# Kernel optimization log

Hardware: AMD Instinct MI355X
Metric: run time of the kernel (lower is better)

The kernel has to match this reference:

```python
import jax, jax.numpy as jnp
import numpy as np

N_HEAD = 12
HEAD_DIM = 64
N_EMBD = 768
ATTN_MULT = 0.125
B, T = 2, 2048
NEG_INF = -1e30


def setup_inputs() -> dict:
    key = jax.random.key(0)
    ks = jax.random.split(key, 3)
    x = jax.random.normal(ks[0], (B, T, N_EMBD), dtype=jnp.float32)
    W_attn = jax.random.normal(ks[1], (N_EMBD, 3 * N_HEAD * HEAD_DIM), dtype=jnp.float32) * 0.02
    b_attn = jnp.zeros((3 * N_HEAD * HEAD_DIM,), dtype=jnp.float32)
    W_proj = jax.random.normal(ks[2], (N_HEAD * HEAD_DIM, N_EMBD), dtype=jnp.float32) * 0.02
    b_proj = jnp.zeros((N_EMBD,), dtype=jnp.float32)
    return {"x": x, "W_attn": W_attn, "b_attn": b_attn, "W_proj": W_proj, "b_proj": b_proj}


def reference(x, W_attn, b_attn, W_proj, b_proj):
    Bsz, Tlen, C = x.shape
    H, D = N_HEAD, HEAD_DIM
    qkv = x @ W_attn + b_attn                       # [B,T,3*H*D]
    q, k, v = jnp.split(qkv, 3, axis=-1)
    q = q.reshape(Bsz, Tlen, H, D).transpose(0, 2, 1, 3)   # [B,H,T,D]
    k = k.reshape(Bsz, Tlen, H, D).transpose(0, 2, 1, 3)
    v = v.reshape(Bsz, Tlen, H, D).transpose(0, 2, 1, 3)

    att = jnp.einsum('bhtd,bhsd->bhts', q, k) * ATTN_MULT  # [B,H,T,T]
    causal = jnp.tril(jnp.ones((Tlen, Tlen), dtype=bool))  # [T,T]
    att = jnp.where(causal, att, NEG_INF)

    # selection mask from head 0 (SelectionHeadLinearComboKind.NONE)
    S = jax.nn.relu(att[:, 0:1, :, :])                     # [B,1,T,T]; relu kills -inf
    # protect_bos_token: zero column 0 (key index 0)
    col = jnp.arange(Tlen)
    S = S * (col[None, None, None, :] != 0)
    # prevent_from_masking_myself: zero diagonal
    S = S * (1.0 - jnp.eye(Tlen, dtype=S.dtype))

    # accumulate selection over query (row) axis: ProtectionKind.NONE
    FF = jnp.cumsum(S, axis=-2)                            # [B,1,T,T]
    att = att - FF                                         # broadcast over heads

    p = jax.nn.softmax(att, axis=-1)                       # [B,H,T,T]
    y = jnp.einsum('bhts,bhsd->bhtd', p, v)                # [B,H,T,D]
    y = y.transpose(0, 2, 1, 3).reshape(Bsz, Tlen, H * D)  # [B,T,H*D]
    return y @ W_proj + b_proj
```

## Files before the change

### kernel.cpp

```cpp
#include <hip/hip_runtime.h>
#include <math.h>

#define T 2048
#define NH 12
#define HD 64
#define C3 2304
#define CE 768
#define NB 2

typedef __attribute__((ext_vector_type(8))) short bf16x8;
typedef __attribute__((ext_vector_type(4))) float f32x4;

__device__ inline void bf16split(float a, unsigned short& h, unsigned short& l) {
    unsigned int u = __float_as_uint(a);
    unsigned int r = (u + 0x7FFFu + ((u >> 16) & 1u)) >> 16;
    h = (unsigned short)r;
    float hf = __uint_as_float(r << 16);
    float lo = a - hf;
    unsigned int v = __float_as_uint(lo);
    l = (unsigned short)((v + 0x7FFFu + ((v >> 16) & 1u)) >> 16);
}

__global__ __launch_bounds__(256) void cvt_split_kernel(const float* __restrict__ A,
        unsigned short* __restrict__ H, unsigned short* __restrict__ L) {
    int i = blockIdx.x * 256 + threadIdx.x;
    float4 a0 = *(reinterpret_cast<const float4*>(A) + (size_t)i * 2);
    float4 a1 = *(reinterpret_cast<const float4*>(A) + (size_t)i * 2 + 1);
    float f[8] = {a0.x, a0.y, a0.z, a0.w, a1.x, a1.y, a1.z, a1.w};
    unsigned short h[8], l[8];
    #pragma unroll
    for (int j = 0; j < 8; ++j) bf16split(f[j], h[j], l[j]);
    uint4 hv, lv;
    hv.x = (unsigned)h[0] | ((unsigned)h[1] << 16); hv.y = (unsigned)h[2] | ((unsigned)h[3] << 16);
    hv.z = (unsigned)h[4] | ((unsigned)h[5] << 16); hv.w = (unsigned)h[6] | ((unsigned)h[7] << 16);
    lv.x = (unsigned)l[0] | ((unsigned)l[1] << 16); lv.y = (unsigned)l[2] | ((unsigned)l[3] << 16);
    lv.z = (unsigned)l[4] | ((unsigned)l[5] << 16); lv.w = (unsigned)l[6] | ((unsigned)l[7] << 16);
    reinterpret_cast<uint4*>(H)[i] = hv;
    reinterpret_cast<uint4*>(L)[i] = lv;
}

__global__ __launch_bounds__(256) void cvt_split_T_kernel(const float* __restrict__ W,
        unsigned short* __restrict__ H, unsigned short* __restrict__ L, int K, int N) {
    __shared__ float tile[64][65];
    const int n0 = blockIdx.x * 64, k0 = blockIdx.y * 64;
    const int t = threadIdx.x;
    {
        int r = t >> 2, c4 = (t & 3) * 16;
        #pragma unroll
        for (int u = 0; u < 4; ++u) {
            float4 w = *reinterpret_cast<const float4*>(&W[(size_t)(k0 + r) * N + n0 + c4 + u * 4]);
            tile[r][c4 + u * 4 + 0] = w.x; tile[r][c4 + u * 4 + 1] = w.y;
            tile[r][c4 + u * 4 + 2] = w.z; tile[r][c4 + u * 4 + 3] = w.w;
        }
    }
    __syncthreads();
    {
        int n = t >> 2, kc = (t & 3) * 16;
        unsigned short h[16], l[16];
        #pragma unroll
        for (int j = 0; j < 16; ++j) bf16split(tile[kc + j][n], h[j], l[j]);
        uint4 hv0, hv1, lv0, lv1;
        hv0.x = (unsigned)h[0] | ((unsigned)h[1] << 16);  hv0.y = (unsigned)h[2] | ((unsigned)h[3] << 16);
        hv0.z = (unsigned)h[4] | ((unsigned)h[5] << 16);  hv0.w = (unsigned)h[6] | ((unsigned)h[7] << 16);
        hv1.x = (unsigned)h[8] | ((unsigned)h[9] << 16);  hv1.y = (unsigned)h[10] | ((unsigned)h[11] << 16);
        hv1.z = (unsigned)h[12] | ((unsigned)h[13] << 16); hv1.w = (unsigned)h[14] | ((unsigned)h[15] << 16);
        lv0.x = (unsigned)l[0] | ((unsigned)l[1] << 16);  lv0.y = (unsigned)l[2] | ((unsigned)l[3] << 16);
        lv0.z = (unsigned)l[4] | ((unsigned)l[5] << 16);  lv0.w = (unsigned)l[6] | ((unsigned)l[7] << 16);
        lv1.x = (unsigned)l[8] | ((unsigned)l[9] << 16);  lv1.y = (unsigned)l[10] | ((unsigned)l[11] << 16);
        lv1.z = (unsigned)l[12] | ((unsigned)l[13] << 16); lv1.w = (unsigned)l[14] | ((unsigned)l[15] << 16);
        size_t o = (size_t)(n0 + n) * K + k0 + kc;
        reinterpret_cast<uint4*>(&H[o])[0] = hv0; reinterpret_cast<uint4*>(&H[o])[1] = hv1;
        reinterpret_cast<uint4*>(&L[o])[0] = lv0; reinterpret_cast<uint4*>(&L[o])[1] = lv1;
    }
}

__global__ __launch_bounds__(256) void cvt_kv_k_kernel(const float* __restrict__ qkv,
        unsigned short* __restrict__ Kh, unsigned short* __restrict__ Kl) {
    int t = blockIdx.x * 256 + threadIdx.x;
    int dg = t & 7;
    int s = (t >> 3) & (T - 1);
    int bh = t >> 14;
    int b = bh / NH, h = bh % NH;
    const float* src = qkv + (size_t)(b * T + s) * C3 + 768 + h * 64 + dg * 8;
    float4 a0 = *reinterpret_cast<const float4*>(src);
    float4 a1 = *reinterpret_cast<const float4*>(src + 4);
    float f[8] = {a0.x, a0.y, a0.z, a0.w, a1.x, a1.y, a1.z, a1.w};
    unsigned short hh[8], ll[8];
    #pragma unroll
    for (int j = 0; j < 8; ++j) bf16split(f[j], hh[j], ll[j]);
    uint4 hv, lv;
    hv.x = (unsigned)hh[0] | ((unsigned)hh[1] << 16); hv.y = (unsigned)hh[2] | ((unsigned)hh[3] << 16);
    hv.z = (unsigned)hh[4] | ((unsigned)hh[5] << 16); hv.w = (unsigned)hh[6] | ((unsigned)hh[7] << 16);
    lv.x = (unsigned)ll[0] | ((unsigned)ll[1] << 16); lv.y = (unsigned)ll[2] | ((unsigned)ll[3] << 16);
    lv.z = (unsigned)ll[4] | ((unsigned)ll[5] << 16); lv.w = (unsigned)ll[6] | ((unsigned)ll[7] << 16);
    size_t o = ((size_t)bh * T + s) * 64 + dg * 8;
    *reinterpret_cast<uint4*>(&Kh[o]) = hv;
    *reinterpret_cast<uint4*>(&Kl[o]) = lv;
}

__global__ __launch_bounds__(256) void cvt_kv_vt_kernel(const float* __restrict__ qkv,
        unsigned short* __restrict__ Vh, unsigned short* __restrict__ Vl) {
    __shared__ float tile[64][65];
    const int s0 = blockIdx.x * 64;
    const int bh = blockIdx.y;
    const int b = bh / NH, h = bh % NH;
    const int tid = threadIdx.x;
    {
        int r = tid >> 2, c0 = (tid & 3) * 16;
        const float* src = qkv + (size_t)(b * T + s0 + r) * C3 + 1536 + h * 64 + c0;
        #pragma unroll
        for (int u = 0; u < 4; ++u) {
            float4 w = *reinterpret_cast<const float4*>(src + u * 4);
            tile[r][c0 + u * 4 + 0] = w.x; tile[r][c0 + u * 4 + 1] = w.y;
            tile[r][c0 + u * 4 + 2] = w.z; tile[r][c0 + u * 4 + 3] = w.w;
        }
    }
    __syncthreads();
    {
        int d = tid >> 2, cs = (tid & 3) * 16;
        unsigned short hh[16], ll[16];
        #pragma unroll
        for (int j = 0; j < 16; ++j) bf16split(tile[cs + j][d], hh[j], ll[j]);
        uint4 hv0, hv1, lv0, lv1;
        hv0.x = (unsigned)hh[0] | ((unsigned)hh[1] << 16);  hv0.y = (unsigned)hh[2] | ((unsigned)hh[3] << 16);
        hv0.z = (unsigned)hh[4] | ((unsigned)hh[5] << 16);  hv0.w = (unsigned)hh[6] | ((unsigned)hh[7] << 16);
        hv1.x = (unsigned)hh[8] | ((unsigned)hh[9] << 16);  hv1.y = (unsigned)hh[10] | ((unsigned)hh[11] << 16);
        hv1.z = (unsigned)hh[12] | ((unsigned)hh[13] << 16); hv1.w = (unsigned)hh[14] | ((unsigned)hh[15] << 16);
        lv0.x = (unsigned)ll[0] | ((unsigned)ll[1] << 16);  lv0.y = (unsigned)ll[2] | ((unsigned)ll[3] << 16);
        lv0.z = (unsigned)ll[4] | ((unsigned)ll[5] << 16);  lv0.w = (unsigned)ll[6] | ((unsigned)ll[7] << 16);
        lv1.x = (unsigned)ll[8] | ((unsigned)ll[9] << 16);  lv1.y = (unsigned)ll[10] | ((unsigned)ll[11] << 16);
        lv1.z = (unsigned)ll[12] | ((unsigned)ll[13] << 16); lv1.w = (unsigned)ll[14] | ((unsigned)ll[15] << 16);
        size_t o = ((size_t)bh * 64 + d) * T + s0 + cs;
        reinterpret_cast<uint4*>(&Vh[o])[0] = hv0; reinterpret_cast<uint4*>(&Vh[o])[1] = hv1;
        reinterpret_cast<uint4*>(&Vl[o])[0] = lv0; reinterpret_cast<uint4*>(&Vl[o])[1] = lv1;
    }
}

#define LDST 40
__global__ __launch_bounds__(256) void gemm_mfma_kernel(
        const unsigned short* __restrict__ Ah, const unsigned short* __restrict__ Al,
        const unsigned short* __restrict__ Bh, const unsigned short* __restrict__ Bl,
        const float* __restrict__ bias, float* __restrict__ Cm,
        int M, int N, int K) {
    __shared__ unsigned short lA[2][128 * LDST];
    __shared__ unsigned short lB[2][128 * LDST];
    const int tid = threadIdx.x;
    const int bm = blockIdx.y * 128, bn = blockIdx.x * 128;
    const int lane = tid & 63, wid = tid >> 6;
    const int wr = wid >> 1, wc = wid & 1;
    f32x4 acc[4][4];
    #pragma unroll
    for (int i = 0; i < 4; ++i)
        #pragma unroll
        for (int j = 0; j < 4; ++j) acc[i][j] = (f32x4){0.f, 0.f, 0.f, 0.f};
    const int srow = tid >> 2, sk8 = (tid & 3) * 8;
    const int arb = wr * 64 + (lane & 15);
    const int brb = wc * 64 + (lane & 15);
    const int koff = (lane >> 4) * 8;
    for (int k0 = 0; k0 < K; k0 += 32) {
        __syncthreads();
        #pragma unroll
        for (int c = 0; c < 2; ++c) {
            int row = srow + 64 * c;
            uint4 va = *reinterpret_cast<const uint4*>(&Ah[(size_t)(bm + row) * K + k0 + sk8]);
            uint4 vb = *reinterpret_cast<const uint4*>(&Al[(size_t)(bm + row) * K + k0 + sk8]);
            uint4 vc = *reinterpret_cast<const uint4*>(&Bh[(size_t)(bn + row) * K + k0 + sk8]);
            uint4 vd = *reinterpret_cast<const uint4*>(&Bl[(size_t)(bn + row) * K + k0 + sk8]);
            *reinterpret_cast<uint4*>(&lA[0][row * LDST + sk8]) = va;
            *reinterpret_cast<uint4*>(&lA[1][row * LDST + sk8]) = vb;
            *reinterpret_cast<uint4*>(&lB[0][row * LDST + sk8]) = vc;
            *reinterpret_cast<uint4*>(&lB[1][row * LDST + sk8]) = vd;
        }
        __syncthreads();
        bf16x8 fa[2][4], fb[2][4];
        #pragma unroll
        for (int fi = 0; fi < 4; ++fi) {
            fa[0][fi] = *reinterpret_cast<const bf16x8*>(&lA[0][(arb + fi * 16) * LDST + koff]);
            fa[1][fi] = *reinterpret_cast<const bf16x8*>(&lA[1][(arb + fi * 16) * LDST + koff]);
            fb[0][fi] = *reinterpret_cast<const bf16x8*>(&lB[0][(brb + fi * 16) * LDST + koff]);
            fb[1][fi] = *reinterpret_cast<const bf16x8*>(&lB[1][(brb + fi * 16) * LDST + koff]);
        }
        #pragma unroll
        for (int fi = 0; fi < 4; ++fi)
            #pragma unroll
            for (int fj = 0; fj < 4; ++fj) {
                acc[fi][fj] = __builtin_amdgcn_mfma_f32_16x16x32_bf16(fa[0][fi], fb[0][fj], acc[fi][fj], 0, 0, 0);
                acc[fi][fj] = __builtin_amdgcn_mfma_f32_16x16x32_bf16(fa[0][fi], fb[1][fj], acc[fi][fj], 0, 0, 0);
                acc[fi][fj] = __builtin_amdgcn_mfma_f32_16x16x32_bf16(fa[1][fi], fb[0][fj], acc[fi][fj], 0, 0, 0);
            }
    }
    #pragma unroll
    for (int fj = 0; fj < 4; ++fj) {
        int col = bn + wc * 64 + fj * 16 + (lane & 15);
        float bv = bias[col];
        #pragma unroll
        for (int fi = 0; fi < 4; ++fi) {
            int row0 = bm + wr * 64 + fi * 16 + (lane >> 4) * 4;
            #pragma unroll
            for (int p = 0; p < 4; ++p)
                Cm[(size_t)(row0 + p) * N + col] = acc[fi][fj][p] + bv;
        }
    }
}

__global__ __launch_bounds__(256) void gemm_bias_kernel(
        const float* __restrict__ A, const float* __restrict__ B,
        const float* __restrict__ bias, float* __restrict__ Cm,
        int M, int N, int K) {
    __shared__ float As[16][64];
    __shared__ float Bs[16][68];
    const int tid = threadIdx.x;
    const int ty = tid >> 4, tx = tid & 15;
    const int bm = blockIdx.y * 64, bn = blockIdx.x * 64;
    float acc[4][4] = {};
    for (int k0 = 0; k0 < K; k0 += 16) {
        {
            int r = tid >> 2;
            int kk = (tid & 3) * 4;
            float4 a = *reinterpret_cast<const float4*>(&A[(size_t)(bm + r) * K + k0 + kk]);
            As[kk + 0][r] = a.x; As[kk + 1][r] = a.y; As[kk + 2][r] = a.z; As[kk + 3][r] = a.w;
        }
        {
            int kk = tid >> 4;
            int c = (tid & 15) * 4;
            *reinterpret_cast<float4*>(&Bs[kk][c]) =
                *reinterpret_cast<const float4*>(&B[(size_t)(k0 + kk) * N + bn + c]);
        }
        __syncthreads();
        #pragma unroll
        for (int kk = 0; kk < 16; ++kk) {
            float4 a4 = *reinterpret_cast<const float4*>(&As[kk][ty * 4]);
            float4 b4 = *reinterpret_cast<const float4*>(&Bs[kk][tx * 4]);
            float av[4] = {a4.x, a4.y, a4.z, a4.w};
            float bv[4] = {b4.x, b4.y, b4.z, b4.w};
            #pragma unroll
            for (int i = 0; i < 4; ++i)
                #pragma unroll
                for (int j = 0; j < 4; ++j)
                    acc[i][j] = fmaf(av[i], bv[j], acc[i][j]);
        }
        __syncthreads();
    }
    #pragma unroll
    for (int i = 0; i < 4; ++i) {
        int row = bm + ty * 4 + i;
        #pragma unroll
        for (int j = 0; j < 4; ++j) {
            int col = bn + tx * 4 + j;
            Cm[(size_t)row * N + col] = acc[i][j] + bias[col];
        }
    }
}

__global__ __launch_bounds__(256) void s0_kernel(const float* __restrict__ qkv,
                                                 float* __restrict__ S) {
    const int kb = blockIdx.x * 64, qb = blockIdx.y * 64, b = blockIdx.z;
    const int tid = threadIdx.x, ty = tid >> 4, tx = tid & 15;
    float* Sb = S + (size_t)b * T * T;
    if (kb > qb) {
        #pragma unroll
        for (int i = 0; i < 4; ++i) {
            int row = qb + ty * 4 + i;
            float4 z = {0.f, 0.f, 0.f, 0.f};
            *reinterpret_cast<float4*>(&Sb[(size_t)row * T + kb + tx * 4]) = z;
        }
        return;
    }
    __shared__ float Qt[64][68];
    __shared__ float Kt[64][68];
    {
        int r = tid >> 2;
        int c0 = (tid & 3) * 16;
        const float* qrow = qkv + (size_t)(b * T + qb + r) * C3 + 0;
        const float* krow = qkv + (size_t)(b * T + kb + r) * C3 + 768;
        #pragma unroll
        for (int u = 0; u < 4; ++u) {
            float4 q4 = *reinterpret_cast<const float4*>(&qrow[c0 + u * 4]);
            float4 k4 = *reinterpret_cast<const float4*>(&krow[c0 + u * 4]);
            int d = c0 + u * 4;
            Qt[d + 0][r] = q4.x; Qt[d + 1][r] = q4.y; Qt[d + 2][r] = q4.z; Qt[d + 3][r] = q4.w;
            Kt[d + 0][r] = k4.x; Kt[d + 1][r] = k4.y; Kt[d + 2][r] = k4.z; Kt[d + 3][r] = k4.w;
        }
    }
    __syncthreads();
    float acc[4][4] = {};
    #pragma unroll
    for (int d = 0; d < 64; ++d) {
        float4 qv = *reinterpret_cast<const float4*>(&Qt[d][ty * 4]);
        float4 kv = *reinterpret_cast<const float4*>(&Kt[d][tx * 4]);
        float qa[4] = {qv.x, qv.y, qv.z, qv.w};
        float ka[4] = {kv.x, kv.y, kv.z, kv.w};
        #pragma unroll
        for (int i = 0; i < 4; ++i)
            #pragma unroll
            for (int j = 0; j < 4; ++j)
                acc[i][j] = fmaf(qa[i], ka[j], acc[i][j]);
    }
    #pragma unroll
    for (int i = 0; i < 4; ++i) {
        int t = qb + ty * 4 + i;
        float o[4];
        #pragma unroll
        for (int j = 0; j < 4; ++j) {
            int s = kb + tx * 4 + j;
            float v = acc[i][j] * 0.125f;
            o[j] = (s >= 1 && s < t) ? fmaxf(v, 0.0f) : 0.0f;
        }
        float4 o4 = {o[0], o[1], o[2], o[3]};
        *reinterpret_cast<float4*>(&Sb[(size_t)t * T + kb + tx * 4]) = o4;
    }
}

__global__ __launch_bounds__(256) void colsum_kernel(const float* __restrict__ S,
                                                     float* __restrict__ Psum) {
    int s = blockIdx.x * 256 + threadIdx.x;
    int j = blockIdx.y, b = blockIdx.z;
    const float* Sb = S + (size_t)b * T * T;
    float sum = 0.f;
    for (int r = 0; r < 64; ++r) sum += Sb[(size_t)(j * 64 + r) * T + s];
    Psum[((size_t)b * 32 + j) * T + s] = sum;
}

__global__ __launch_bounds__(256) void scanseg_kernel(float* __restrict__ Psum) {
    int s = blockIdx.x * 256 + threadIdx.x;
    int b = blockIdx.y;
    float run = 0.f;
    for (int j = 0; j < 32; ++j) {
        size_t idx = ((size_t)b * 32 + j) * T + s;
        float v = Psum[idx];
        Psum[idx] = run;
        run += v;
    }
}

__global__ __launch_bounds__(256) void ffscan_kernel(float* __restrict__ S,
                                                     const float* __restrict__ Psum) {
    int s = blockIdx.x * 256 + threadIdx.x;
    int j = blockIdx.y, b = blockIdx.z;
    float run = Psum[((size_t)b * 32 + j) * T + s];
    float* Sb = S + (size_t)b * T * T;
    for (int r = 0; r < 64; ++r) {
        size_t idx = (size_t)(j * 64 + r) * T + s;
        run += Sb[idx];
        Sb[idx] = run;
    }
}

#define FST 72
__global__ __launch_bounds__(256) void flash_mfma_kernel(
        const float* __restrict__ qkv,
        const unsigned short* __restrict__ Kh, const unsigned short* __restrict__ Kl,
        const unsigned short* __restrict__ Vth, const unsigned short* __restrict__ Vtl,
        const float* __restrict__ FF, float* __restrict__ Y,
        float* __restrict__ PO, float* __restrict__ PML, int split) {
    const int hb = blockIdx.x;
    const int h = hb % NH, b = hb / NH;
    int qt, kt0, kt1, mode;
    if (split) {
        const int u = blockIdx.y;
        if (u < 16)      { qt = 16 + u; kt0 = 0;  kt1 = 16;     mode = 1; }
        else if (u < 32) { qt = 31 - u; kt0 = 0;  kt1 = qt + 1; mode = 0; }
        else             { qt = 63 - u; kt0 = 16; kt1 = qt + 1; mode = 2; }
    } else {
        qt = 31 - blockIdx.y; kt0 = 0; kt1 = qt + 1; mode = 0;
    }
    const int qb = qt * 64;
    const int tid = threadIdx.x;
    const int lane = tid & 63, w = tid >> 6;
    const int fr = lane & 15, fg = lane >> 4;
    __shared__ unsigned short KP[2][64 * FST];
    __shared__ unsigned short Vt[2][64 * FST];

    bf16x8 qh[2], ql[2];
    #pragma unroll
    for (int ks = 0; ks < 2; ++ks) {
        const float* qp = qkv + (size_t)(b * T + qb + w * 16 + fr) * C3 + h * 64 + ks * 32 + fg * 8;
        float4 q0 = *reinterpret_cast<const float4*>(qp);
        float4 q1 = *reinterpret_cast<const float4*>(qp + 4);
        float qf[8] = {q0.x, q0.y, q0.z, q0.w, q1.x, q1.y, q1.z, q1.w};
        #pragma unroll
        for (int e = 0; e < 8; ++e) {
            unsigned short hh, ll;
            bf16split(qf[e], hh, ll);
            qh[ks][e] = (short)hh; ql[ks][e] = (short)ll;
        }
    }

    float m[4], l[4];
    f32x4 Oacc[4];
    #pragma unroll
    for (int p = 0; p < 4; ++p) { m[p] = -1e30f; l[p] = 0.f; }
    #pragma unroll
    for (int fd = 0; fd < 4; ++fd) Oacc[fd] = (f32x4){0.f, 0.f, 0.f, 0.f};

    const float* FFb = FF + (size_t)b * T * T;
    const int sr = tid >> 2, sc0 = (tid & 3) * 16;

    for (int kt = kt0; kt < kt1; ++kt) {
        const int kb = kt * 64;
        __syncthreads();
        {
            const unsigned short* ksrc = Kh + ((size_t)hb * T + kb + sr) * 64 + sc0;
            const unsigned short* ksrl = Kl + ((size_t)hb * T + kb + sr) * 64 + sc0;
            const unsigned short* vsrc = Vth + ((size_t)hb * 64 + sr) * T + kb + sc0;
            const unsigned short* vsrl = Vtl + ((size_t)hb * 64 + sr) * T + kb + sc0;
            uint4 k0v = reinterpret_cast<const uint4*>(ksrc)[0];
            uint4 k1v = reinterpret_cast<const uint4*>(ksrc)[1];
            uint4 k2v = reinterpret_cast<const uint4*>(ksrl)[0];
            uint4 k3v = reinterpret_cast<const uint4*>(ksrl)[1];
            uint4 v0v = reinterpret_cast<const uint4*>(vsrc)[0];
            uint4 v1v = reinterpret_cast<const uint4*>(vsrc)[1];
            uint4 v2v = reinterpret_cast<const uint4*>(vsrl)[0];
            uint4 v3v = reinterpret_cast<const uint4*>(vsrl)[1];
            *reinterpret_cast<uint4*>(&KP[0][sr * FST + sc0 + 0]) = k0v;
            *reinterpret_cast<uint4*>(&KP[0][sr * FST + sc0 + 8]) = k1v;
            *reinterpret_cast<uint4*>(&KP[1][sr * FST + sc0 + 0]) = k2v;
            *reinterpret_cast<uint4*>(&KP[1][sr * FST + sc0 + 8]) = k3v;
            *reinterpret_cast<uint4*>(&Vt[0][sr * FST + sc0 + 0]) = v0v;
            *reinterpret_cast<uint4*>(&Vt[0][sr * FST + sc0 + 8]) = v1v;
            *reinterpret_cast<uint4*>(&Vt[1][sr * FST + sc0 + 0]) = v2v;
            *reinterpret_cast<uint4*>(&Vt[1][sr * FST + sc0 + 8]) = v3v;
        }
        __syncthreads();
        f32x4 qk[4];
        #pragma unroll
        for (int fj = 0; fj < 4; ++fj) qk[fj] = (f32x4){0.f, 0.f, 0.f, 0.f};
        #pragma unroll
        for (int ks = 0; ks < 2; ++ks) {
            bf16x8 kbh[4], kbl[4];
            #pragma unroll
            for (int fj = 0; fj < 4; ++fj) {
                kbh[fj] = *reinterpret_cast<const bf16x8*>(&KP[0][(fj * 16 + fr) * FST + ks * 32 + fg * 8]);
                kbl[fj] = *reinterpret_cast<const bf16x8*>(&KP[1][(fj * 16 + fr) * FST + ks * 32 + fg * 8]);
            }
            #pragma unroll
            for (int fj = 0; fj < 4; ++fj) {
                qk[fj] = __builtin_amdgcn_mfma_f32_16x16x32_bf16(qh[ks], kbh[fj], qk[fj], 0, 0, 0);
                qk[fj] = __builtin_amdgcn_mfma_f32_16x16x32_bf16(qh[ks], kbl[fj], qk[fj], 0, 0, 0);
                qk[fj] = __builtin_amdgcn_mfma_f32_16x16x32_bf16(ql[ks], kbh[fj], qk[fj], 0, 0, 0);
            }
        }
        float sc[4][4];
        #pragma unroll
        for (int p = 0; p < 4; ++p) {
            int t = qb + w * 16 + fg * 4 + p;
            #pragma unroll
            for (int fj = 0; fj < 4; ++fj) {
                int s = kb + fj * 16 + fr;
                float v = qk[fj][p] * 0.125f - FFb[(size_t)t * T + s];
                sc[fj][p] = (s <= t) ? v : -1e30f;
            }
        }
        #pragma unroll
        for (int p = 0; p < 4; ++p) {
            float tm = fmaxf(fmaxf(sc[0][p], sc[1][p]), fmaxf(sc[2][p], sc[3][p]));
            tm = fmaxf(tm, __shfl_xor(tm, 1));
            tm = fmaxf(tm, __shfl_xor(tm, 2));
            tm = fmaxf(tm, __shfl_xor(tm, 4));
            tm = fmaxf(tm, __shfl_xor(tm, 8));
            float mn = fmaxf(m[p], tm);
            float scale = __expf(m[p] - mn);
            float rs = 0.f;
            #pragma unroll
            for (int fj = 0; fj < 4; ++fj) {
                float pe = __expf(sc[fj][p] - mn);
                sc[fj][p] = pe; rs += pe;
            }
            rs += __shfl_xor(rs, 1); rs += __shfl_xor(rs, 2);
            rs += __shfl_xor(rs, 4); rs += __shfl_xor(rs, 8);
            l[p] = l[p] * scale + rs;
            m[p] = mn;
            #pragma unroll
            for (int fd = 0; fd < 4; ++fd) Oacc[fd][p] *= scale;
        }
        __syncthreads();
        #pragma unroll
        for (int p = 0; p < 4; ++p) {
            int qrow = w * 16 + fg * 4 + p;
            #pragma unroll
            for (int fj = 0; fj < 4; ++fj) {
                unsigned short hh, ll;
                bf16split(sc[fj][p], hh, ll);
                KP[0][qrow * FST + fj * 16 + fr] = hh;
                KP[1][qrow * FST + fj * 16 + fr] = ll;
            }
        }
        __syncthreads();
        #pragma unroll
        for (int ks = 0; ks < 2; ++ks) {
            bf16x8 pah = *reinterpret_cast<const bf16x8*>(&KP[0][(w * 16 + fr) * FST + ks * 32 + fg * 8]);
            bf16x8 pal = *reinterpret_cast<const bf16x8*>(&KP[1][(w * 16 + fr) * FST + ks * 32 + fg * 8]);
            bf16x8 vbh[4], vbl[4];
            #pragma unroll
            for (int fd = 0; fd < 4; ++fd) {
                vbh[fd] = *reinterpret_cast<const bf16x8*>(&Vt[0][(fd * 16 + fr) * FST + ks * 32 + fg * 8]);
                vbl[fd] = *reinterpret_cast<const bf16x8*>(&Vt[1][(fd * 16 + fr) * FST + ks * 32 + fg * 8]);
            }
            #pragma unroll
            for (int fd = 0; fd < 4; ++fd) {
                Oacc[fd] = __builtin_amdgcn_mfma_f32_16x16x32_bf16(pah, vbh[fd], Oacc[fd], 0, 0, 0);
                Oacc[fd] = __builtin_amdgcn_mfma_f32_16x16x32_bf16(pah, vbl[fd], Oacc[fd], 0, 0, 0);
                Oacc[fd] = __builtin_amdgcn_mfma_f32_16x16x32_bf16(pal, vbh[fd], Oacc[fd], 0, 0, 0);
            }
        }
    }
    if (mode == 0) {
        #pragma unroll
        for (int p = 0; p < 4; ++p) {
            int t = qb + w * 16 + fg * 4 + p;
            float inv = 1.f / l[p];
            float* Yrow = Y + (size_t)(b * T + t) * CE + h * 64;
            #pragma unroll
            for (int fd = 0; fd < 4; ++fd)
                Yrow[fd * 16 + fr] = Oacc[fd][p] * inv;
        }
    } else {
        const int pidx = (b * NH + h) * 16 + (qt - 16);
        float* Ob  = PO  + (size_t)(mode - 1) * (NB * NH * 16 * 4096) + (size_t)pidx * 4096;
        float* mlb = PML + (size_t)(mode - 1) * (NB * NH * 16 * 128)  + (size_t)pidx * 128;
        #pragma unroll
        for (int p = 0; p < 4; ++p) {
            int rr = w * 16 + fg * 4 + p;
            #pragma unroll
            for (int fd = 0; fd < 4; ++fd)
                Ob[rr * 64 + fd * 16 + fr] = Oacc[fd][p];
            if (fr == 0) { mlb[rr] = m[p]; mlb[64 + rr] = l[p]; }
        }
    }
}

__global__ __launch_bounds__(256) void flash_kernel(const float* __restrict__ qkv,
                                                    const float* __restrict__ FF,
                                                    float* __restrict__ Y,
                                                    float* __restrict__ PO,
                                                    float* __restrict__ PML,
                                                    int split) {
    const int hb = blockIdx.x;
    const int h = hb % NH, b = hb / NH;
    int qt, kt0, kt1, mode;
    if (split) {
        const int u = blockIdx.y;
        if (u < 16)      { qt = 16 + u; kt0 = 0;  kt1 = 16;     mode = 1; }
        else if (u < 32) { qt = 31 - u; kt0 = 0;  kt1 = qt + 1; mode = 0; }
        else             { qt = 63 - u; kt0 = 16; kt1 = qt + 1; mode = 2; }
    } else {
        qt = 31 - blockIdx.y; kt0 = 0; kt1 = qt + 1; mode = 0;
    }
    const int qb = qt * 64;
    const int tid = threadIdx.x, ty = tid >> 4, tx = tid & 15;
    __shared__ float Qt[64][68];
    __shared__ float KtPs[64][68];
    __shared__ float Vs[64][68];
    const int r = tid >> 2, c0 = (tid & 3) * 16;
    {
        const float* qrow = qkv + (size_t)(b * T + qb + r) * C3 + h * 64;
        #pragma unroll
        for (int u = 0; u < 4; ++u) {
            float4 q4 = *reinterpret_cast<const float4*>(&qrow[c0 + u * 4]);
            int d = c0 + u * 4;
            Qt[d + 0][r] = q4.x; Qt[d + 1][r] = q4.y; Qt[d + 2][r] = q4.z; Qt[d + 3][r] = q4.w;
        }
    }
    float m[4], l[4], O[4][4];
    #pragma unroll
    for (int i = 0; i < 4; ++i) {
        m[i] = -1e30f; l[i] = 0.f;
        #pragma unroll
        for (int j = 0; j < 4; ++j) O[i][j] = 0.f;
    }
    const float* FFb = FF + (size_t)b * T * T;
    for (int kt = kt0; kt < kt1; ++kt) {
        const int kb = kt * 64;
        __syncthreads();
        {
            const float* krow = qkv + (size_t)(b * T + kb + r) * C3 + 768 + h * 64;
            const float* vrow = qkv + (size_t)(b * T + kb + r) * C3 + 1536 + h * 64;
            #pragma unroll
            for (int u = 0; u < 4; ++u) {
                float4 k4 = *reinterpret_cast<const float4*>(&krow[c0 + u * 4]);
                int d = c0 + u * 4;
                KtPs[d + 0][r] = k4.x; KtPs[d + 1][r] = k4.y;
                KtPs[d + 2][r] = k4.z; KtPs[d + 3][r] = k4.w;
                *reinterpret_cast<float4*>(&Vs[r][c0 + u * 4]) =
                    *reinterpret_cast<const float4*>(&vrow[c0 + u * 4]);
            }
        }
        __syncthreads();
        float sc[4][4] = {};
        #pragma unroll
        for (int d = 0; d < 64; ++d) {
            float4 qv = *reinterpret_cast<const float4*>(&Qt[d][ty * 4]);
            float4 kv = *reinterpret_cast<const float4*>(&KtPs[d][tx * 4]);
            float qa[4] = {qv.x, qv.y, qv.z, qv.w};
            float ka[4] = {kv.x, kv.y, kv.z, kv.w};
            #pragma unroll
            for (int i = 0; i < 4; ++i)
                #pragma unroll
                for (int j = 0; j < 4; ++j)
                    sc[i][j] = fmaf(qa[i], ka[j], sc[i][j]);
        }
        #pragma unroll
        for (int i = 0; i < 4; ++i) {
            int t = qb + ty * 4 + i;
            float4 f4 = *reinterpret_cast<const float4*>(&FFb[(size_t)t * T + kb + tx * 4]);
            float fv[4] = {f4.x, f4.y, f4.z, f4.w};
            #pragma unroll
            for (int j = 0; j < 4; ++j) {
                int s = kb + tx * 4 + j;
                float v = sc[i][j] * 0.125f - fv[j];
                sc[i][j] = (s <= t) ? v : -1e30f;
            }
        }
        #pragma unroll
        for (int i = 0; i < 4; ++i) {
            float tm = fmaxf(fmaxf(sc[i][0], sc[i][1]), fmaxf(sc[i][2], sc[i][3]));
            tm = fmaxf(tm, __shfl_xor(tm, 1));
            tm = fmaxf(tm, __shfl_xor(tm, 2));
            tm = fmaxf(tm, __shfl_xor(tm, 4));
            tm = fmaxf(tm, __shfl_xor(tm, 8));
            float mn = fmaxf(m[i], tm);
            float scale = __expf(m[i] - mn);
            float rs = 0.f;
            #pragma unroll
            for (int j = 0; j < 4; ++j) {
                float p = __expf(sc[i][j] - mn);
                sc[i][j] = p; rs += p;
            }
            rs += __shfl_xor(rs, 1); rs += __shfl_xor(rs, 2);
            rs += __shfl_xor(rs, 4); rs += __shfl_xor(rs, 8);
            l[i] = l[i] * scale + rs;
            m[i] = mn;
            #pragma unroll
            for (int j = 0; j < 4; ++j) O[i][j] *= scale;
        }
        __syncthreads();
        #pragma unroll
        for (int i = 0; i < 4; ++i) {
            float4 p4 = {sc[i][0], sc[i][1], sc[i][2], sc[i][3]};
            *reinterpret_cast<float4*>(&KtPs[ty * 4 + i][tx * 4]) = p4;
        }
        __syncthreads();
        #pragma unroll
        for (int j4 = 0; j4 < 16; ++j4) {
            float pv[4][4];
            #pragma unroll
            for (int i = 0; i < 4; ++i) {
                float4 t4 = *reinterpret_cast<const float4*>(&KtPs[ty * 4 + i][j4 * 4]);
                pv[i][0] = t4.x; pv[i][1] = t4.y; pv[i][2] = t4.z; pv[i][3] = t4.w;
            }
            #pragma unroll
            for (int jj = 0; jj < 4; ++jj) {
                float4 v4 = *reinterpret_cast<const float4*>(&Vs[j4 * 4 + jj][tx * 4]);
                float vv[4] = {v4.x, v4.y, v4.z, v4.w};
                #pragma unroll
                for (int i = 0; i < 4; ++i)
                    #pragma unroll
                    for (int dd = 0; dd < 4; ++dd)
                        O[i][dd] = fmaf(pv[i][jj], vv[dd], O[i][dd]);
            }
        }
    }
    if (mode == 0) {
        #pragma unroll
        for (int i = 0; i < 4; ++i) {
            int t = qb + ty * 4 + i;
            float inv = 1.f / l[i];
            float4 o4 = {O[i][0] * inv, O[i][1] * inv, O[i][2] * inv, O[i][3] * inv};
            *reinterpret_cast<float4*>(&Y[(size_t)(b * T + t) * CE + h * 64 + tx * 4]) = o4;
        }
    } else {
        const int pidx = (b * NH + h) * 16 + (qt - 16);
        float* Ob  = PO  + (size_t)(mode - 1) * (NB * NH * 16 * 4096) + (size_t)pidx * 4096;
        float* mlb = PML + (size_t)(mode - 1) * (NB * NH * 16 * 128)  + (size_t)pidx * 128;
        #pragma unroll
        for (int i = 0; i < 4; ++i) {
            int rr = ty * 4 + i;
            float4 o4 = {O[i][0], O[i][1], O[i][2], O[i][3]};
            *reinterpret_cast<float4*>(&Ob[rr * 64 + tx * 4]) = o4;
            if (tx == 0) { mlb[rr] = m[i]; mlb[64 + rr] = l[i]; }
        }
    }
}

__global__ __launch_bounds__(256) void merge_kernel(const float* __restrict__ PO,
                                                    const float* __restrict__ PML,
                                                    float* __restrict__ Y) {
    const int p = blockIdx.x;
    const int q16 = p & 15;
    const int hb = p >> 4;
    const int h = hb % NH, b = hb / NH;
    const int qt = 16 + q16;
    const float* O0  = PO  + (size_t)p * 4096;
    const float* O1  = PO  + (size_t)(NB * NH * 16) * 4096 + (size_t)p * 4096;
    const float* ml0 = PML + (size_t)p * 128;
    const float* ml1 = PML + (size_t)(NB * NH * 16) * 128  + (size_t)p * 128;
    const int tid = threadIdx.x;
    const int r = tid >> 2, c0 = (tid & 3) * 16;
    float m0 = ml0[r], l0 = ml0[64 + r];
    float m1 = ml1[r], l1 = ml1[64 + r];
    float M  = fmaxf(m0, m1);
    float a0 = __expf(m0 - M), a1 = __expf(m1 - M);
    float inv = 1.f / (a0 * l0 + a1 * l1);
    const int t = qt * 64 + r;
    float* Yrow = Y + (size_t)(b * T + t) * CE + h * 64;
    #pragma unroll
    for (int u = 0; u < 4; ++u) {
        float4 x0 = *reinterpret_cast<const float4*>(&O0[r * 64 + c0 + u * 4]);
        float4 x1 = *reinterpret_cast<const float4*>(&O1[r * 64 + c0 + u * 4]);
        float4 y;
        y.x = (a0 * x0.x + a1 * x1.x) * inv;
        y.y = (a0 * x0.y + a1 * x1.y) * inv;
        y.z = (a0 * x0.z + a1 * x1.z) * inv;
        y.w = (a0 * x0.w + a1 * x1.w) * inv;
        *reinterpret_cast<float4*>(&Yrow[c0 + u * 4]) = y;
    }
}

extern "C" void kernel_launch(void* const* d_in, const int* in_sizes, int n_in,
                              void* d_out, int out_size, void* d_ws, size_t ws_size,
                              hipStream_t stream) {
    const float* x      = (const float*)d_in[0];
    const float* W_attn = (const float*)d_in[1];
    const float* b_attn = (const float*)d_in[2];
    const float* W_proj = (const float*)d_in[3];
    const float* b_proj = (const float*)d_in[4];
    float* out = (float*)d_out;

    char* ws = (char*)d_ws;
    const size_t QKV_BYTES = (size_t)NB * T * C3 * 4;
    const size_t S_BYTES   = (size_t)NB * T * T * 4;
    const size_t P_BYTES   = (size_t)NB * 32 * T * 4;
    const size_t Y_BYTES   = (size_t)NB * T * CE * 4;
    const size_t PO_BYTES  = (size_t)2 * NB * NH * 16 * 4096 * 4;
    const size_t PML_BYTES = (size_t)2 * NB * NH * 16 * 128 * 4;
    const size_t PLANE_X   = (size_t)NB * T * CE * 2;
    const size_t PLANE_WA  = (size_t)C3 * CE * 2;
    const size_t PLANE_WP  = (size_t)CE * CE * 2;
    const size_t PLANE_KV  = (size_t)NB * NH * T * 64 * 2;

    const size_t U_OFF  = QKV_BYTES + S_BYTES + P_BYTES + Y_BYTES;
    const size_t U_SIZE = PO_BYTES + PML_BYTES;
    const size_t W_OFF  = U_OFF + U_SIZE;
    const size_t KV_OFF = W_OFF + 2 * PLANE_WA + 2 * PLANE_WP;

    float* qkv  = (float*)ws;
    float* S    = (float*)(ws + QKV_BYTES);
    float* Psum = (float*)(ws + QKV_BYTES + S_BYTES);
    float* Yb   = (float*)(ws + QKV_BYTES + S_BYTES + P_BYTES);
    float* PO   = (float*)(ws + U_OFF);
    float* PML  = (float*)(ws + U_OFF + PO_BYTES);
    unsigned short* Xh  = (unsigned short*)(ws + U_OFF);
    unsigned short* Xl  = (unsigned short*)(ws + U_OFF + PLANE_X);
    unsigned short* Yh  = Xh;
    unsigned short* Yl  = Xl;
    unsigned short* WAh = (unsigned short*)(ws + W_OFF);
    unsigned short* WAl = (unsigned short*)(ws + W_OFF + PLANE_WA);
    unsigned short* WPh = (unsigned short*)(ws + W_OFF + 2 * PLANE_WA);
    unsigned short* WPl = (unsigned short*)(ws + W_OFF + 2 * PLANE_WA + PLANE_WP);
    unsigned short* Khp = (unsigned short*)(ws + KV_OFF);
    unsigned short* Klp = (unsigned short*)(ws + KV_OFF + PLANE_KV);
    unsigned short* VTh = (unsigned short*)(ws + KV_OFF + 2 * PLANE_KV);
    unsigned short* VTl = (unsigned short*)(ws + KV_OFF + 3 * PLANE_KV);

    const size_t NEED_SPLIT = U_OFF + U_SIZE;
    const size_t NEED_MFMA  = KV_OFF;
    const size_t NEED_KV    = KV_OFF + 4 * PLANE_KV;
    const int split = (ws_size >= NEED_SPLIT) ? 1 : 0;
    const int mfma  = (ws_size >= NEED_MFMA) ? 1 : 0;
    const int kv    = (ws_size >= NEED_KV) ? 1 : 0;

    const int M = NB * T;

    if (mfma) {
        cvt_split_T_kernel<<<dim3(C3 / 64, CE / 64), 256, 0, stream>>>(W_attn, WAh, WAl, CE, C3);
        cvt_split_T_kernel<<<dim3(CE / 64, CE / 64), 256, 0, stream>>>(W_proj, WPh, WPl, CE, CE);
        cvt_split_kernel<<<dim3((M * CE / 8) / 256), 256, 0, stream>>>(x, Xh, Xl);
        gemm_mfma_kernel<<<dim3(C3 / 128, M / 128), 256, 0, stream>>>(Xh, Xl, WAh, WAl, b_attn, qkv, M, C3, CE);
    } else {
        gemm_bias_kernel<<<dim3(C3 / 64, M / 64), 256, 0, stream>>>(x, W_attn, b_attn, qkv, M, C3, CE);
    }
    s0_kernel<<<dim3(T / 64, T / 64, NB), 256, 0, stream>>>(qkv, S);
    colsum_kernel<<<dim3(T / 256, 32, NB), 256, 0, stream>>>(S, Psum);
    scanseg_kernel<<<dim3(T / 256, NB), 256, 0, stream>>>(Psum);
    ffscan_kernel<<<dim3(T / 256, 32, NB), 256, 0, stream>>>(S, Psum);
    if (kv) {
        cvt_kv_k_kernel<<<dim3((NB * NH * T * 8) / 256), 256, 0, stream>>>(qkv, Khp, Klp);
        cvt_kv_vt_kernel<<<dim3(T / 64, NB * NH), 256, 0, stream>>>(qkv, VTh, VTl);
        if (split) {
            flash_mfma_kernel<<<dim3(NB * NH, 48), 256, 0, stream>>>(qkv, Khp, Klp, VTh, VTl, S, Yb, PO, PML, 1);
            merge_kernel<<<dim3(NB * NH * 16), 256, 0, stream>>>(PO, PML, Yb);
        } else {
            flash_mfma_kernel<<<dim3(NB * NH, 32), 256, 0, stream>>>(qkv, Khp, Klp, VTh, VTl, S, Yb, PO, PML, 0);
        }
    } else if (split) {
        flash_kernel<<<dim3(NB * NH, 48), 256, 0, stream>>>(qkv, S, Yb, PO, PML, 1);
        merge_kernel<<<dim3(NB * NH * 16), 256, 0, stream>>>(PO, PML, Yb);
    } else {
        flash_kernel<<<dim3(NB * NH, 32), 256, 0, stream>>>(qkv, S, Yb, PO, PML, 0);
    }
    if (mfma) {
        cvt_split_kernel<<<dim3((M * CE / 8) / 256), 256, 0, stream>>>(Yb, Yh, Yl);
        gemm_mfma_kernel<<<dim3(CE / 128, M / 128), 256, 0, stream>>>(Yh, Yl, WPh, WPl, b_proj, out, M, CE, CE);
    } else {
        gemm_bias_kernel<<<dim3(CE / 64, M / 64), 256, 0, stream>>>(Yb, W_proj, b_proj, out, M, CE, CE);
    }
}
```

Baseline: 293.2 us.

## Precompute Q bf16 split, use MFMA for head-0 scores, finer flash KV chunking

```diff
diff --git a/kernel.cpp b/kernel.cpp
--- a/kernel.cpp
+++ b/kernel.cpp
@@ -74,28 +74,39 @@
     }
 }
 
-__global__ __launch_bounds__(256) void cvt_kv_k_kernel(const float* __restrict__ qkv,
+__global__ __launch_bounds__(256) void cvt_qk_kernel(const float* __restrict__ qkv,
+        unsigned short* __restrict__ Qh, unsigned short* __restrict__ Ql,
         unsigned short* __restrict__ Kh, unsigned short* __restrict__ Kl) {
     int t = blockIdx.x * 256 + threadIdx.x;
     int dg = t & 7;
     int s = (t >> 3) & (T - 1);
     int bh = t >> 14;
     int b = bh / NH, h = bh % NH;
-    const float* src = qkv + (size_t)(b * T + s) * C3 + 768 + h * 64 + dg * 8;
-    float4 a0 = *reinterpret_cast<const float4*>(src);
-    float4 a1 = *reinterpret_cast<const float4*>(src + 4);
-    float f[8] = {a0.x, a0.y, a0.z, a0.w, a1.x, a1.y, a1.z, a1.w};
-    unsigned short hh[8], ll[8];
-    #pragma unroll
-    for (int j = 0; j < 8; ++j) bf16split(f[j], hh[j], ll[j]);
-    uint4 hv, lv;
-    hv.x = (unsigned)hh[0] | ((unsigned)hh[1] << 16); hv.y = (unsigned)hh[2] | ((unsigned)hh[3] << 16);
-    hv.z = (unsigned)hh[4] | ((unsigned)hh[5] << 16); hv.w = (unsigned)hh[6] | ((unsigned)hh[7] << 16);
-    lv.x = (unsigned)ll[0] | ((unsigned)ll[1] << 16); lv.y = (unsigned)ll[2] | ((unsigned)ll[3] << 16);
-    lv.z = (unsigned)ll[4] | ((unsigned)ll[5] << 16); lv.w = (unsigned)ll[6] | ((unsigned)ll[7] << 16);
+    const float* qs = qkv + (size_t)(b * T + s) * C3 + h * 64 + dg * 8;
+    const float* ks = qs + 768;
     size_t o = ((size_t)bh * T + s) * 64 + dg * 8;
-    *reinterpret_cast<uint4*>(&Kh[o]) = hv;
-    *reinterpret_cast<uint4*>(&Kl[o]) = lv;
+    #pragma unroll
+    for (int which = 0; which < 2; ++which) {
+        const float* src = (which == 0) ? qs : ks;
+        float4 a0 = *reinterpret_cast<const float4*>(src);
+        float4 a1 = *reinterpret_cast<const float4*>(src + 4);
+        float f[8] = {a0.x, a0.y, a0.z, a0.w, a1.x, a1.y, a1.z, a1.w};
+        unsigned short hh[8], ll[8];
+        #pragma unroll
+        for (int j = 0; j < 8; ++j) bf16split(f[j], hh[j], ll[j]);
+        uint4 hv, lv;
+        hv.x = (unsigned)hh[0] | ((unsigned)hh[1] << 16); hv.y = (unsigned)hh[2] | ((unsigned)hh[3] << 16);
+        hv.z = (unsigned)hh[4] | ((unsigned)hh[5] << 16); hv.w = (unsigned)hh[6] | ((unsigned)hh[7] << 16);
+        lv.x = (unsigned)ll[0] | ((unsigned)ll[1] << 16); lv.y = (unsigned)ll[2] | ((unsigned)ll[3] << 16);
+        lv.z = (unsigned)ll[4] | ((unsigned)ll[5] << 16); lv.w = (unsigned)ll[6] | ((unsigned)ll[7] << 16);
+        if (which == 0) {
+            *reinterpret_cast<uint4*>(&Qh[o]) = hv;
+            *reinterpret_cast<uint4*>(&Ql[o]) = lv;
+        } else {
+            *reinterpret_cast<uint4*>(&Kh[o]) = hv;
+            *reinterpret_cast<uint4*>(&Kl[o]) = lv;
+        }
+    }
 }
 
 __global__ __launch_bounds__(256) void cvt_kv_vt_kernel(const float* __restrict__ qkv,
@@ -252,6 +263,79 @@
     }
 }
 
+#define FST 72
+
+__global__ __launch_bounds__(256) void s0_mfma_kernel(
+        const unsigned short* __restrict__ Qh, const unsigned short* __restrict__ Ql,
+        const unsigned short* __restrict__ Kh, const unsigned short* __restrict__ Kl,
+        float* __restrict__ S) {
+    const int kb = blockIdx.x * 64, qb = blockIdx.y * 64, b = blockIdx.z;
+    const int tid = threadIdx.x;
+    float* Sb = S + (size_t)b * T * T;
+    if (kb > qb) {
+        const int ty = tid >> 4, tx = tid & 15;
+        #pragma unroll
+        for (int i = 0; i < 4; ++i) {
+            float4 z = {0.f, 0.f, 0.f, 0.f};
+            *reinterpret_cast<float4*>(&Sb[(size_t)(qb + ty * 4 + i) * T + kb + tx * 4]) = z;
+        }
+        return;
+    }
+    const int lane = tid & 63, w = tid >> 6;
+    const int fr = lane & 15, fg = lane >> 4;
+    __shared__ unsigned short Ks[2][64 * FST];
+    const int hb0 = b * NH;
+    {
+        const int sr = tid >> 2, sc0 = (tid & 3) * 16;
+        const unsigned short* kh = Kh + ((size_t)hb0 * T + kb + sr) * 64 + sc0;
+        const unsigned short* kl = Kl + ((size_t)hb0 * T + kb + sr) * 64 + sc0;
+        uint4 a0 = reinterpret_cast<const uint4*>(kh)[0];
+        uint4 a1 = reinterpret_cast<const uint4*>(kh)[1];
+        uint4 b0 = reinterpret_cast<const uint4*>(kl)[0];
+        uint4 b1 = reinterpret_cast<const uint4*>(kl)[1];
+        *reinterpret_cast<uint4*>(&Ks[0][sr * FST + sc0 + 0]) = a0;
+        *reinterpret_cast<uint4*>(&Ks[0][sr * FST + sc0 + 8]) = a1;
+        *reinterpret_cast<uint4*>(&Ks[1][sr * FST + sc0 + 0]) = b0;
+        *reinterpret_cast<uint4*>(&Ks[1][sr * FST + sc0 + 8]) = b1;
+    }
+    bf16x8 qh[2], ql[2];
+    #pragma unroll
+    for (int ks = 0; ks < 2; ++ks) {
+        size_t qo = ((size_t)hb0 * T + qb + w * 16 + fr) * 64 + ks * 32 + fg * 8;
+        qh[ks] = *reinterpret_cast<const bf16x8*>(&Qh[qo]);
+        ql[ks] = *reinterpret_cast<const bf16x8*>(&Ql[qo]);
+    }
+    __syncthreads();
+    f32x4 qk[4];
+    #pragma unroll
+    for (int fj = 0; fj < 4; ++fj) qk[fj] = (f32x4){0.f, 0.f, 0.f, 0.f};
+    #pragma unroll
+    for (int ks = 0; ks < 2; ++ks) {
+        bf16x8 kbh[4], kbl[4];
+        #pragma unroll
+        for (int fj = 0; fj < 4; ++fj) {
+            kbh[fj] = *reinterpret_cast<const bf16x8*>(&Ks[0][(fj * 16 + fr) * FST + ks * 32 + fg * 8]);
+            kbl[fj] = *reinterpret_cast<const bf16x8*>(&Ks[1][(fj * 16 + fr) * FST + ks * 32 + fg * 8]);
+        }
+        #pragma unroll
+        for (int fj = 0; fj < 4; ++fj) {
+            qk[fj] = __builtin_amdgcn_mfma_f32_16x16x32_bf16(qh[ks], kbh[fj], qk[fj], 0, 0, 0);
+            qk[fj] = __builtin_amdgcn_mfma_f32_16x16x32_bf16(qh[ks], kbl[fj], qk[fj], 0, 0, 0);
+            qk[fj] = __builtin_amdgcn_mfma_f32_16x16x32_bf16(ql[ks], kbh[fj], qk[fj], 0, 0, 0);
+        }
+    }
+    #pragma unroll
+    for (int p = 0; p < 4; ++p) {
+        int t = qb + w * 16 + fg * 4 + p;
+        #pragma unroll
+        for (int fj = 0; fj < 4; ++fj) {
+            int s = kb + fj * 16 + fr;
+            float v = qk[fj][p] * 0.125f;
+            Sb[(size_t)t * T + s] = (s >= 1 && s < t) ? fmaxf(v, 0.0f) : 0.0f;
+        }
+    }
+}
+
 __global__ __launch_bounds__(256) void s0_kernel(const float* __restrict__ qkv,
                                                  float* __restrict__ S) {
     const int kb = blockIdx.x * 64, qb = blockIdx.y * 64, b = blockIdx.z;
@@ -346,23 +430,42 @@
     }
 }
 
-#define FST 72
+__device__ inline int chunk_base_fn(int qt) {
+    int base = 0;
+    for (int q = 8; q < qt; ++q) base += (q + 8) >> 3;
+    return base;
+}
+
 __global__ __launch_bounds__(256) void flash_mfma_kernel(
-        const float* __restrict__ qkv,
+        const unsigned short* __restrict__ Qh, const unsigned short* __restrict__ Ql,
         const unsigned short* __restrict__ Kh, const unsigned short* __restrict__ Kl,
         const unsigned short* __restrict__ Vth, const unsigned short* __restrict__ Vtl,
         const float* __restrict__ FF, float* __restrict__ Y,
-        float* __restrict__ PO, float* __restrict__ PML, int split) {
+        float* __restrict__ PART) {
     const int hb = blockIdx.x;
     const int h = hb % NH, b = hb / NH;
-    int qt, kt0, kt1, mode;
-    if (split) {
-        const int u = blockIdx.y;
-        if (u < 16)      { qt = 16 + u; kt0 = 0;  kt1 = 16;     mode = 1; }
-        else if (u < 32) { qt = 31 - u; kt0 = 0;  kt1 = qt + 1; mode = 0; }
-        else             { qt = 63 - u; kt0 = 16; kt1 = qt + 1; mode = 2; }
-    } else {
-        qt = 31 - blockIdx.y; kt0 = 0; kt1 = qt + 1; mode = 0;
+    int qt = 0, kt0 = 0, kt1 = 1;
+    {
+        int u = blockIdx.y, cnt = 0;
+        bool found = false;
+        for (int sz = 8; sz >= 1 && !found; --sz) {
+            for (int q = 31; q >= 0; --q) {
+                int nch = (q + 8) >> 3;
+                int nfull = nch - 1;
+                int last = q + 1 - 8 * nfull;
+                int nthis = ((sz == 8) ? nfull : 0) + ((last == sz) ? 1 : 0);
+                if (u < cnt + nthis) {
+                    int off = u - cnt;
+                    qt = q;
+                    int ci = (sz == 8 && off < nfull) ? off : nfull;
+                    kt0 = ci * 8;
+                    kt1 = (ci == nfull) ? (q + 1) : (kt0 + 8);
+                    found = true;
+                    break;
+                }
+                cnt += nthis;
+            }
+        }
     }
     const int qb = qt * 64;
     const int tid = threadIdx.x;
@@ -374,16 +477,9 @@
     bf16x8 qh[2], ql[2];
     #pragma unroll
     for (int ks = 0; ks < 2; ++ks) {
-        const float* qp = qkv + (size_t)(b * T + qb + w * 16 + fr) * C3 + h * 64 + ks * 32 + fg * 8;
-        float4 q0 = *reinterpret_cast<const float4*>(qp);
-        float4 q1 = *reinterpret_cast<const float4*>(qp + 4);
-        float qf[8] = {q0.x, q0.y, q0.z, q0.w, q1.x, q1.y, q1.z, q1.w};
-        #pragma unroll
-        for (int e = 0; e < 8; ++e) {
-            unsigned short hh, ll;
-            bf16split(qf[e], hh, ll);
-            qh[ks][e] = (short)hh; ql[ks][e] = (short)ll;
-        }
+        size_t qo = ((size_t)hb * T + qb + w * 16 + fr) * 64 + ks * 32 + fg * 8;
+        qh[ks] = *reinterpret_cast<const bf16x8*>(&Qh[qo]);
+        ql[ks] = *reinterpret_cast<const bf16x8*>(&Ql[qo]);
     }
 
     float m[4], l[4];
@@ -422,6 +518,14 @@
             *reinterpret_cast<uint4*>(&Vt[1][sr * FST + sc0 + 8]) = v3v;
         }
         __syncthreads();
+        float ffv[4][4];
+        #pragma unroll
+        for (int p = 0; p < 4; ++p) {
+            int t = qb + w * 16 + fg * 4 + p;
+            #pragma unroll
+            for (int fj = 0; fj < 4; ++fj)
+                ffv[p][fj] = FFb[(size_t)t * T + kb + fj * 16 + fr];
+        }
         f32x4 qk[4];
         #pragma unroll
         for (int fj = 0; fj < 4; ++fj) qk[fj] = (f32x4){0.f, 0.f, 0.f, 0.f};
@@ -447,7 +551,7 @@
             #pragma unroll
             for (int fj = 0; fj < 4; ++fj) {
                 int s = kb + fj * 16 + fr;
-                float v = qk[fj][p] * 0.125f - FFb[(size_t)t * T + s];
+                float v = qk[fj][p] * 0.125f - ffv[p][fj];
                 sc[fj][p] = (s <= t) ? v : -1e30f;
             }
         }
@@ -504,7 +608,7 @@
             }
         }
     }
-    if (mode == 0) {
+    if (qt < 8) {
         #pragma unroll
         for (int p = 0; p < 4; ++p) {
             int t = qb + w * 16 + fg * 4 + p;
@@ -515,17 +619,59 @@
                 Yrow[fd * 16 + fr] = Oacc[fd][p] * inv;
         }
     } else {
-        const int pidx = (b * NH + h) * 16 + (qt - 16);
-        float* Ob  = PO  + (size_t)(mode - 1) * (NB * NH * 16 * 4096) + (size_t)pidx * 4096;
-        float* mlb = PML + (size_t)(mode - 1) * (NB * NH * 16 * 128)  + (size_t)pidx * 128;
+        const int cb = chunk_base_fn(qt) + (kt0 >> 3);
+        float* Ob = PART + (size_t)(hb * 72 + cb) * 4224;
         #pragma unroll
         for (int p = 0; p < 4; ++p) {
             int rr = w * 16 + fg * 4 + p;
             #pragma unroll
             for (int fd = 0; fd < 4; ++fd)
                 Ob[rr * 64 + fd * 16 + fr] = Oacc[fd][p];
-            if (fr == 0) { mlb[rr] = m[p]; mlb[64 + rr] = l[p]; }
-        }
+            if (fr == 0) { Ob[4096 + rr] = m[p]; Ob[4096 + 64 + rr] = l[p]; }
+        }
+    }
+}
+
+__global__ __launch_bounds__(256) void merge8_kernel(const float* __restrict__ PART,
+                                                     float* __restrict__ Y) {
+    const int hb = blockIdx.x;
+    const int qt = 8 + blockIdx.y;
+    const int h = hb % NH, b = hb / NH;
+    const int nch = (qt + 8) >> 3;
+    const float* base = PART + (size_t)(hb * 72 + chunk_base_fn(qt)) * 4224;
+    const int tid = threadIdx.x;
+    const int r = tid >> 2, c0 = (tid & 3) * 16;
+    float mm[4], ll[4];
+    float M = -1e30f;
+    #pragma unroll
+    for (int c = 0; c < 4; ++c) {
+        int cc = (c < nch) ? c : 0;
+        float mv = base[(size_t)cc * 4224 + 4096 + r];
+        float lv = base[(size_t)cc * 4224 + 4096 + 64 + r];
+        mm[c] = (c < nch) ? mv : -1e30f;
+        ll[c] = (c < nch) ? lv : 0.f;
+        M = fmaxf(M, mm[c]);
+    }
+    float a[4], L = 0.f;
+    #pragma unroll
+    for (int c = 0; c < 4; ++c) {
+        a[c] = (c < nch) ? __expf(mm[c] - M) : 0.f;
+        L += a[c] * ll[c];
+    }
+    float inv = 1.f / L;
+    const int t = qt * 64 + r;
+    float* Yrow = Y + (size_t)(b * T + t) * CE + h * 64;
+    #pragma unroll
+    for (int u = 0; u < 4; ++u) {
+        float ax = 0.f, ay = 0.f, az = 0.f, aw = 0.f;
+        #pragma unroll
+        for (int c = 0; c < 4; ++c) {
+            int cc = (c < nch) ? c : 0;
+            float4 xo = *reinterpret_cast<const float4*>(&base[(size_t)cc * 4224 + r * 64 + c0 + u * 4]);
+            ax += a[c] * xo.x; ay += a[c] * xo.y; az += a[c] * xo.z; aw += a[c] * xo.w;
+        }
+        float4 y = {ax * inv, ay * inv, az * inv, aw * inv};
+        *reinterpret_cast<float4*>(&Yrow[c0 + u * 4]) = y;
     }
 }
 
@@ -751,6 +897,8 @@
     float* PML  = (float*)(ws + U_OFF + PO_BYTES);
     unsigned short* Xh  = (unsigned short*)(ws + U_OFF);
     unsigned short* Xl  = (unsigned short*)(ws + U_OFF + PLANE_X);
+    unsigned short* Qhp = Xh;
+    unsigned short* Qlp = Xl;
     unsigned short* Yh  = Xh;
     unsigned short* Yl  = Xl;
     unsigned short* WAh = (unsigned short*)(ws + W_OFF);
@@ -761,13 +909,14 @@
     unsigned short* Klp = (unsigned short*)(ws + KV_OFF + PLANE_KV);
     unsigned short* VTh = (unsigned short*)(ws + KV_OFF + 2 * PLANE_KV);
     unsigned short* VTl = (unsigned short*)(ws + KV_OFF + 3 * PLANE_KV);
+    float* PART = qkv;
 
     const size_t NEED_SPLIT = U_OFF + U_SIZE;
     const size_t NEED_MFMA  = KV_OFF;
     const size_t NEED_KV    = KV_OFF + 4 * PLANE_KV;
     const int split = (ws_size >= NEED_SPLIT) ? 1 : 0;
     const int mfma  = (ws_size >= NEED_MFMA) ? 1 : 0;
-    const int kv    = (ws_size >= NEED_KV) ? 1 : 0;
+    const int kv    = (ws_size >= NEED_KV && mfma) ? 1 : 0;
 
     const int M = NB * T;
 
@@ -779,19 +928,19 @@
     } else {
         gemm_bias_kernel<<<dim3(C3 / 64, M / 64), 256, 0, stream>>>(x, W_attn, b_attn, qkv, M, C3, CE);
     }
-    s0_kernel<<<dim3(T / 64, T / 64, NB), 256, 0, stream>>>(qkv, S);
+    if (kv) {
+        cvt_qk_kernel<<<dim3((NB * NH * T * 8) / 256), 256, 0, stream>>>(qkv, Qhp, Qlp, Khp, Klp);
+        cvt_kv_vt_kernel<<<dim3(T / 64, NB * NH), 256, 0, stream>>>(qkv, VTh, VTl);
+        s0_mfma_kernel<<<dim3(T / 64, T / 64, NB), 256, 0, stream>>>(Qhp, Qlp, Khp, Klp, S);
+    } else {
+        s0_kernel<<<dim3(T / 64, T / 64, NB), 256, 0, stream>>>(qkv, S);
+    }
     colsum_kernel<<<dim3(T / 256, 32, NB), 256, 0, stream>>>(S, Psum);
     scanseg_kernel<<<dim3(T / 256, NB), 256, 0, stream>>>(Psum);
     ffscan_kernel<<<dim3(T / 256, 32, NB), 256, 0, stream>>>(S, Psum);
     if (kv) {
-        cvt_kv_k_kernel<<<dim3((NB * NH * T * 8) / 256), 256, 0, stream>>>(qkv, Khp, Klp);
-        cvt_kv_vt_kernel<<<dim3(T / 64, NB * NH), 256, 0, stream>>>(qkv, VTh, VTl);
-        if (split) {
-            flash_mfma_kernel<<<dim3(NB * NH, 48), 256, 0, stream>>>(qkv, Khp, Klp, VTh, VTl, S, Yb, PO, PML, 1);
-            merge_kernel<<<dim3(NB * NH * 16), 256, 0, stream>>>(PO, PML, Yb);
-        } else {
-            flash_mfma_kernel<<<dim3(NB * NH, 32), 256, 0, stream>>>(qkv, Khp, Klp, VTh, VTl, S, Yb, PO, PML, 0);
-        }
+        flash_mfma_kernel<<<dim3(NB * NH, 80), 256, 0, stream>>>(Qhp, Qlp, Khp, Klp, VTh, VTl, S, Yb, PART);
+        merge8_kernel<<<dim3(NB * NH, 24), 256, 0, stream>>>(PART, Yb);
     } else if (split) {
         flash_kernel<<<dim3(NB * NH, 48), 256, 0, stream>>>(qkv, S, Yb, PO, PML, 1);
         merge_kernel<<<dim3(NB * NH * 16), 256, 0, stream>>>(PO, PML, Yb);
```

Measured after the change: 296.5 us. About the same (+1.1%).
